# Kernel optimization log

Measured on AMD Instinct MI355X. Metric: run time of the kernel, lower is better.

Reference implementation:

```python
import jax, jax.numpy as jnp
import numpy as np


def setup_inputs() -> dict:
    key = jax.random.key(0)
    k1, k2, k3 = jax.random.split(key, 3)
    B, T, D, K = 8, 1024, 384, 4
    z = jax.random.normal(k1, (B, T, D), dtype=jnp.float32)
    gt_dT = jax.random.normal(k2, (B, T, T, K), dtype=jnp.float32)
    sigma = jax.random.uniform(k3, (K,), dtype=jnp.float32, minval=0.25, maxval=1.0)
    return {"z": z, "gt_dT": gt_dT, "sigma": sigma}


def reference(z, gt_dT, sigma):
    # Pairwise squared distances via ||a-b||^2 = ||a||^2 + ||b||^2 - 2 a.b
    # (same math as the naive [B,T,T,D] expansion, without materializing it).
    sq = jnp.sum(z * z, axis=-1)                      # [B, T]
    gram = jnp.einsum("btd,bsd->bts", z, z)           # [B, T, T]
    dist2 = sq[:, :, None] + sq[:, None, :] - 2.0 * gram
    # Gaussian kernel weight from ground-truth patch-transform deltas.
    kernel = jnp.sum(gt_dT * gt_dT / (2.0 * sigma * sigma), axis=-1)  # [B, T, T]
    w = jnp.exp(-kernel)
    loss = jnp.mean(w * dist2)
    return loss
```

## Files before the change

### kernel.cpp

```cpp
#include <hip/hip_runtime.h>
#include <hip/hip_bf16.h>


typedef float  f32x4   __attribute__((ext_vector_type(4)));
typedef short  bf16x8  __attribute__((ext_vector_type(8)));
typedef unsigned short ushort4_t __attribute__((ext_vector_type(4)));

#define T_DIM 1024
#define D_DIM 384
#define BK    192
#define LDK   200

__device__ __forceinline__ unsigned short f32_bf16(float f) {
    unsigned int u = __float_as_uint(f);
    u += 0x7FFFu + ((u >> 16) & 1u);
    return (unsigned short)(u >> 16);
}

__global__ void prep_sq(const float* __restrict__ z, float* __restrict__ sq) {
    int row  = blockIdx.x;
    int lane = threadIdx.x;
    const float* zr = z + (size_t)row * D_DIM;
    float s = 0.f;
#pragma unroll
    for (int q = 0; q < 6; ++q) {
        float x = zr[lane + 64 * q];
        s += x * x;
    }
#pragma unroll
    for (int off = 32; off; off >>= 1) s += __shfl_down(s, off);
    if (lane == 0) sq[row] = s;
}

__launch_bounds__(256, 2)
__global__ void tile_loss(const float* __restrict__ z,
                          const float* __restrict__ gt,
                          const float* __restrict__ sigma,
                          const float* __restrict__ sq,
                          float* __restrict__ partials) {
    __shared__ unsigned short Alds[64 * LDK];
    __shared__ unsigned short Blds[64 * LDK];
    __shared__ float sqA[64], sqB[64], red[4];

    const int bid = blockIdx.x;
    const int b   = bid >> 8;
    const int r8  = bid & 255;
    const int t0  = (r8 >> 4) * 64;
    const int s0  = (r8 & 15) * 64;

    const int tid  = threadIdx.x;
    const int lane = tid & 63, wid = tid >> 6;
    const int wr = wid >> 1, wc = wid & 1;
    const int l15 = lane & 15, lq = lane >> 4;

    float4 g[2][2][4];
#pragma unroll
    for (int mt = 0; mt < 2; ++mt)
#pragma unroll
        for (int nt = 0; nt < 2; ++nt)
#pragma unroll
            for (int r = 0; r < 4; ++r) {
                int t = t0 + wr * 32 + mt * 16 + lq * 4 + r;
                int s = s0 + wc * 32 + nt * 16 + l15;
                g[mt][nt][r] = *(const float4*)(gt +
                    ((((size_t)b << 10) + t) * T_DIM + (size_t)s) * 4);
            }

    if (tid < 64)       sqA[tid]      = sq[(b << 10) + t0 + tid];
    else if (tid < 128) sqB[tid - 64] = sq[(b << 10) + s0 + (tid - 64)];

    const float* Asrc = z + (((size_t)b << 10) + t0) * D_DIM;
    const float* Bsrc = z + (((size_t)b << 10) + s0) * D_DIM;

    f32x4 acc[2][2] = {};

    for (int kc = 0; kc < 2; ++kc) {
        const int k0 = kc * BK;
        for (int i = tid; i < 3072; i += 256) {
            int row = i / 48, c4 = (i % 48) * 4;
            float4 av = *(const float4*)&Asrc[row * D_DIM + k0 + c4];
            float4 bv = *(const float4*)&Bsrc[row * D_DIM + k0 + c4];
            ushort4_t ah = { f32_bf16(av.x), f32_bf16(av.y), f32_bf16(av.z), f32_bf16(av.w) };
            ushort4_t bh = { f32_bf16(bv.x), f32_bf16(bv.y), f32_bf16(bv.z), f32_bf16(bv.w) };
            *(ushort4_t*)&Alds[row * LDK + c4] = ah;
            *(ushort4_t*)&Blds[row * LDK + c4] = bh;
        }
        __syncthreads();
#pragma unroll
        for (int k = 0; k < BK; k += 32) {
            bf16x8 a0 = *(const bf16x8*)&Alds[(wr * 32 +      l15) * LDK + k + lq * 8];
            bf16x8 a1 = *(const bf16x8*)&Alds[(wr * 32 + 16 + l15) * LDK + k + lq * 8];
            bf16x8 b0 = *(const bf16x8*)&Blds[(wc * 32 +      l15) * LDK + k + lq * 8];
            bf16x8 b1 = *(const bf16x8*)&Blds[(wc * 32 + 16 + l15) * LDK + k + lq * 8];
            acc[0][0] = __builtin_amdgcn_mfma_f32_16x16x32_bf16(a0, b0, acc[0][0], 0, 0, 0);
            acc[0][1] = __builtin_amdgcn_mfma_f32_16x16x32_bf16(a0, b1, acc[0][1], 0, 0, 0);
            acc[1][0] = __builtin_amdgcn_mfma_f32_16x16x32_bf16(a1, b0, acc[1][0], 0, 0, 0);
            acc[1][1] = __builtin_amdgcn_mfma_f32_16x16x32_bf16(a1, b1, acc[1][1], 0, 0, 0);
        }
        __syncthreads();
    }

    const float i0 = 0.5f / (sigma[0] * sigma[0]);
    const float i1 = 0.5f / (sigma[1] * sigma[1]);
    const float i2 = 0.5f / (sigma[2] * sigma[2]);
    const float i3 = 0.5f / (sigma[3] * sigma[3]);

    float psum = 0.f;
#pragma unroll
    for (int mt = 0; mt < 2; ++mt)
#pragma unroll
        for (int nt = 0; nt < 2; ++nt)
#pragma unroll
            for (int r = 0; r < 4; ++r) {
                int tloc = wr * 32 + mt * 16 + lq * 4 + r;
                int sloc = wc * 32 + nt * 16 + l15;
                float gram = acc[mt][nt][r];
                float d2 = sqA[tloc] + sqB[sloc] - 2.0f * gram;
                float4 gv = g[mt][nt][r];
                float kv = gv.x * gv.x * i0 + gv.y * gv.y * i1
                         + gv.z * gv.z * i2 + gv.w * gv.w * i3;
                psum += __expf(-kv) * d2;
            }

#pragma unroll
    for (int off = 32; off; off >>= 1) psum += __shfl_down(psum, off);
    if (lane == 0) red[wid] = psum;
    __syncthreads();
    if (tid == 0) partials[bid] = red[0] + red[1] + red[2] + red[3];
}

__global__ void final_reduce(const float* __restrict__ partials, float* __restrict__ out) {
    __shared__ float red[4];
    int tid = threadIdx.x;
    float s = 0.f;
    for (int i = tid; i < 2048; i += 256) s += partials[i];
#pragma unroll
    for (int off = 32; off; off >>= 1) s += __shfl_down(s, off);
    int lane = tid & 63, wid = tid >> 6;
    if (lane == 0) red[wid] = s;
    __syncthreads();
    if (tid == 0) out[0] = (red[0] + red[1] + red[2] + red[3]) * (1.0f / 8388608.0f);
}

extern "C" void kernel_launch(void* const* d_in, const int* in_sizes, int n_in,
                              void* d_out, int out_size, void* d_ws, size_t ws_size,
                              hipStream_t stream) {
    const float* z     = (const float*)d_in[0];
    const float* gt    = (const float*)d_in[1];
    const float* sigma = (const float*)d_in[2];
    float* out = (float*)d_out;

    float* sq       = (float*)d_ws;
    float* partials = sq + 8192;

    prep_sq<<<8192, 64, 0, stream>>>(z, sq);
    tile_loss<<<2048, 256, 0, stream>>>(z, gt, sigma, sq, partials);
    final_reduce<<<1, 256, 0, stream>>>(partials, out);
}
```

Measured before the change: 66.35 us.

## Keep A fragments in registers and stream four B tiles per block

Each block now covers 64 rows of t against 256 columns of s, processed as four 64-column sub-tiles. The A operand is converted to bf16 once and held in registers across all sub-tiles. B tiles are staged into a full-depth, XOR-swizzled LDS buffer, and the next tile's B data and gt_dT values are prefetched while the current epilogue runs. The grid drops from 2048 to 512 blocks to cut redundant A loads and conversions, at the cost of fewer blocks for latency hiding, more registers per thread, and two extra barriers per sub-tile.

```diff
diff --git a/kernel.cpp b/kernel.cpp
--- a/kernel.cpp
+++ b/kernel.cpp
@@ -8,8 +8,6 @@
 
 #define T_DIM 1024
 #define D_DIM 384
-#define BK    192
-#define LDK   200
 
 __device__ __forceinline__ unsigned short f32_bf16(float f) {
     unsigned int u = __float_as_uint(f);
@@ -38,93 +36,128 @@
                           const float* __restrict__ sigma,
                           const float* __restrict__ sq,
                           float* __restrict__ partials) {
-    __shared__ unsigned short Alds[64 * LDK];
-    __shared__ unsigned short Blds[64 * LDK];
-    __shared__ float sqA[64], sqB[64], red[4];
+    __shared__ unsigned short Blds[64 * D_DIM];
+    __shared__ float sq_s[T_DIM];
+    __shared__ float red[4];
 
-    const int bid = blockIdx.x;
-    const int b   = bid >> 8;
-    const int r8  = bid & 255;
-    const int t0  = (r8 >> 4) * 64;
-    const int s0  = (r8 & 15) * 64;
+    const int bid   = blockIdx.x;
+    const int b     = bid >> 6;
+    const int tt    = (bid >> 2) & 15;
+    const int sgrp  = bid & 3;
+    const int t0    = tt * 64;
+    const int sbase = sgrp * 256;
 
     const int tid  = threadIdx.x;
-    const int lane = tid & 63, wid = tid >> 6;
-    const int wr = wid >> 1, wc = wid & 1;
-    const int l15 = lane & 15, lq = lane >> 4;
+    const int lane = tid & 63, w = tid >> 6;
+    const int l15  = lane & 15, lq = lane >> 4;
 
-    float4 g[2][2][4];
-#pragma unroll
-    for (int mt = 0; mt < 2; ++mt)
-#pragma unroll
-        for (int nt = 0; nt < 2; ++nt)
-#pragma unroll
-            for (int r = 0; r < 4; ++r) {
-                int t = t0 + wr * 32 + mt * 16 + lq * 4 + r;
-                int s = s0 + wc * 32 + nt * 16 + l15;
-                g[mt][nt][r] = *(const float4*)(gt +
-                    ((((size_t)b << 10) + t) * T_DIM + (size_t)s) * 4);
-            }
-
-    if (tid < 64)       sqA[tid]      = sq[(b << 10) + t0 + tid];
-    else if (tid < 128) sqB[tid - 64] = sq[(b << 10) + s0 + (tid - 64)];
-
-    const float* Asrc = z + (((size_t)b << 10) + t0) * D_DIM;
-    const float* Bsrc = z + (((size_t)b << 10) + s0) * D_DIM;
-
-    f32x4 acc[2][2] = {};
-
-    for (int kc = 0; kc < 2; ++kc) {
-        const int k0 = kc * BK;
-        for (int i = tid; i < 3072; i += 256) {
-            int row = i / 48, c4 = (i % 48) * 4;
-            float4 av = *(const float4*)&Asrc[row * D_DIM + k0 + c4];
-            float4 bv = *(const float4*)&Bsrc[row * D_DIM + k0 + c4];
-            ushort4_t ah = { f32_bf16(av.x), f32_bf16(av.y), f32_bf16(av.z), f32_bf16(av.w) };
-            ushort4_t bh = { f32_bf16(bv.x), f32_bf16(bv.y), f32_bf16(bv.z), f32_bf16(bv.w) };
-            *(ushort4_t*)&Alds[row * LDK + c4] = ah;
-            *(ushort4_t*)&Blds[row * LDK + c4] = bh;
-        }
-        __syncthreads();
-#pragma unroll
-        for (int k = 0; k < BK; k += 32) {
-            bf16x8 a0 = *(const bf16x8*)&Alds[(wr * 32 +      l15) * LDK + k + lq * 8];
-            bf16x8 a1 = *(const bf16x8*)&Alds[(wr * 32 + 16 + l15) * LDK + k + lq * 8];
-            bf16x8 b0 = *(const bf16x8*)&Blds[(wc * 32 +      l15) * LDK + k + lq * 8];
-            bf16x8 b1 = *(const bf16x8*)&Blds[(wc * 32 + 16 + l15) * LDK + k + lq * 8];
-            acc[0][0] = __builtin_amdgcn_mfma_f32_16x16x32_bf16(a0, b0, acc[0][0], 0, 0, 0);
-            acc[0][1] = __builtin_amdgcn_mfma_f32_16x16x32_bf16(a0, b1, acc[0][1], 0, 0, 0);
-            acc[1][0] = __builtin_amdgcn_mfma_f32_16x16x32_bf16(a1, b0, acc[1][0], 0, 0, 0);
-            acc[1][1] = __builtin_amdgcn_mfma_f32_16x16x32_bf16(a1, b1, acc[1][1], 0, 0, 0);
-        }
-        __syncthreads();
-    }
+    const float* zb = z + (size_t)b * T_DIM * D_DIM;
+    char* bb = (char*)Blds;
 
     const float i0 = 0.5f / (sigma[0] * sigma[0]);
     const float i1 = 0.5f / (sigma[1] * sigma[1]);
     const float i2 = 0.5f / (sigma[2] * sigma[2]);
     const float i3 = 0.5f / (sigma[3] * sigma[3]);
 
+    *(float4*)&sq_s[tid * 4] = *(const float4*)&sq[b * T_DIM + tid * 4];
+
+    bf16x8 af[12];
+    {
+        const float* Ar = zb + (size_t)(t0 + w * 16 + l15) * D_DIM + lq * 8;
+#pragma unroll
+        for (int kk = 0; kk < 12; ++kk) {
+            float4 lo = *(const float4*)(Ar + kk * 32);
+            float4 hi = *(const float4*)(Ar + kk * 32 + 4);
+            bf16x8 t;
+            t[0] = (short)f32_bf16(lo.x); t[1] = (short)f32_bf16(lo.y);
+            t[2] = (short)f32_bf16(lo.z); t[3] = (short)f32_bf16(lo.w);
+            t[4] = (short)f32_bf16(hi.x); t[5] = (short)f32_bf16(hi.y);
+            t[6] = (short)f32_bf16(hi.z); t[7] = (short)f32_bf16(hi.w);
+            af[kk] = t;
+        }
+    }
+
+    auto stageB = [&](int s0) {
+#pragma unroll
+        for (int rp = 0; rp < 2; ++rp) {
+            int row = rp * 32 + (tid >> 3);
+            const float* src = zb + (size_t)(s0 + row) * D_DIM + (tid & 7) * 4;
+            int base = row * 768 + (tid & 7) * 8;
+            int sw   = (row & 7) << 4;
+#pragma unroll
+            for (int it = 0; it < 12; ++it) {
+                float4 v = *(const float4*)(src + it * 32);
+                ushort4_t h = { f32_bf16(v.x), f32_bf16(v.y),
+                                f32_bf16(v.z), f32_bf16(v.w) };
+                *(ushort4_t*)(bb + ((base + it * 64) ^ sw)) = h;
+            }
+        }
+    };
+
+    const float* gbase = gt + ((size_t)b << 22);
+    auto loadGT = [&](float4 gg[4][4], int s0) {
+#pragma unroll
+        for (int nt = 0; nt < 4; ++nt)
+#pragma unroll
+            for (int r = 0; r < 4; ++r) {
+                int t = t0 + w * 16 + lq * 4 + r;
+                int s = s0 + nt * 16 + l15;
+                gg[nt][r] = *(const float4*)(gbase + (((size_t)t << 10) + s) * 4);
+            }
+    };
+
+    float4 g[4][4];
+    stageB(sbase);
+    loadGT(g, sbase);
+    __syncthreads();
+
     float psum = 0.f;
 #pragma unroll
-    for (int mt = 0; mt < 2; ++mt)
+    for (int j = 0; j < 4; ++j) {
+        f32x4 acc[4] = {};
 #pragma unroll
-        for (int nt = 0; nt < 2; ++nt)
+        for (int kk = 0; kk < 12; ++kk) {
+#pragma unroll
+            for (int nt = 0; nt < 4; ++nt) {
+                int row = nt * 16 + l15;
+                int off = (row * 768 + kk * 64 + lq * 16) ^ ((row & 7) << 4);
+                bf16x8 bf = *(const bf16x8*)(bb + off);
+                acc[nt] = __builtin_amdgcn_mfma_f32_16x16x32_bf16(af[kk], bf, acc[nt], 0, 0, 0);
+            }
+        }
+        __syncthreads();
+
+        float4 gn[4][4];
+        if (j < 3) {
+            stageB(sbase + (j + 1) * 64);
+            loadGT(gn, sbase + (j + 1) * 64);
+        }
+
+#pragma unroll
+        for (int nt = 0; nt < 4; ++nt)
 #pragma unroll
             for (int r = 0; r < 4; ++r) {
-                int tloc = wr * 32 + mt * 16 + lq * 4 + r;
-                int sloc = wc * 32 + nt * 16 + l15;
-                float gram = acc[mt][nt][r];
-                float d2 = sqA[tloc] + sqB[sloc] - 2.0f * gram;
-                float4 gv = g[mt][nt][r];
+                int tg2 = t0 + w * 16 + lq * 4 + r;
+                int sg2 = sbase + j * 64 + nt * 16 + l15;
+                float d2 = sq_s[tg2] + sq_s[sg2] - 2.0f * acc[nt][r];
+                float4 gv = g[nt][r];
                 float kv = gv.x * gv.x * i0 + gv.y * gv.y * i1
                          + gv.z * gv.z * i2 + gv.w * gv.w * i3;
                 psum += __expf(-kv) * d2;
             }
 
+        if (j < 3) {
+#pragma unroll
+            for (int nt = 0; nt < 4; ++nt)
+#pragma unroll
+                for (int r = 0; r < 4; ++r) g[nt][r] = gn[nt][r];
+            __syncthreads();
+        }
+    }
+
 #pragma unroll
     for (int off = 32; off; off >>= 1) psum += __shfl_down(psum, off);
-    if (lane == 0) red[wid] = psum;
+    if (lane == 0) red[w] = psum;
     __syncthreads();
     if (tid == 0) partials[bid] = red[0] + red[1] + red[2] + red[3];
 }
@@ -132,12 +165,10 @@
 __global__ void final_reduce(const float* __restrict__ partials, float* __restrict__ out) {
     __shared__ float red[4];
     int tid = threadIdx.x;
-    float s = 0.f;
-    for (int i = tid; i < 2048; i += 256) s += partials[i];
+    float s = partials[tid] + partials[tid + 256];
 #pragma unroll
     for (int off = 32; off; off >>= 1) s += __shfl_down(s, off);
-    int lane = tid & 63, wid = tid >> 6;
-    if (lane == 0) red[wid] = s;
+    if ((tid & 63) == 0) red[tid >> 6] = s;
     __syncthreads();
     if (tid == 0) out[0] = (red[0] + red[1] + red[2] + red[3]) * (1.0f / 8388608.0f);
 }
@@ -154,6 +185,6 @@
     float* partials = sq + 8192;
 
     prep_sq<<<8192, 64, 0, stream>>>(z, sq);
-    tile_loss<<<2048, 256, 0, stream>>>(z, gt, sigma, sq, partials);
+    tile_loss<<<512, 256, 0, stream>>>(z, gt, sigma, sq, partials);
     final_reduce<<<1, 256, 0, stream>>>(partials, out);
 }
```

Result: faster. 59.20 us (-10.8%).

## Precompute bf16 z in prep kernel and load MFMA operands directly per wave

Applied to the files above, without the earlier changes.

The prep kernel now also writes a bf16 copy of z, so the tile kernel no longer converts fp32 to bf16 or stages operands through LDS with block-wide barriers. Each wave independently computes a 32x32 tile, reading its MFMA fragments straight from global or L2. gt_dT is loaded with nontemporal loads after the GEMM in an interleaved load and consume schedule, exp is replaced by exp2 with log2e folded into the scales, and partials are reduced per wave. The trade is lost A/B reuse across waves in LDS, more global traffic for z, and an extra write pass for the bf16 copy.

```diff
diff --git a/kernel.cpp b/kernel.cpp
--- a/kernel.cpp
+++ b/kernel.cpp
@@ -4,12 +4,9 @@
 
 typedef float  f32x4   __attribute__((ext_vector_type(4)));
 typedef short  bf16x8  __attribute__((ext_vector_type(8)));
-typedef unsigned short ushort4_t __attribute__((ext_vector_type(4)));
 
 #define T_DIM 1024
 #define D_DIM 384
-#define BK    192
-#define LDK   200
 
 __device__ __forceinline__ unsigned short f32_bf16(float f) {
     unsigned int u = __float_as_uint(f);
@@ -17,15 +14,18 @@
     return (unsigned short)(u >> 16);
 }
 
-__global__ void prep_sq(const float* __restrict__ z, float* __restrict__ sq) {
+__global__ void prep(const float* __restrict__ z, float* __restrict__ sq,
+                     unsigned short* __restrict__ zbf) {
     int row  = blockIdx.x;
     int lane = threadIdx.x;
     const float* zr = z + (size_t)row * D_DIM;
+    unsigned short* zo = zbf + (size_t)row * D_DIM;
     float s = 0.f;
 #pragma unroll
     for (int q = 0; q < 6; ++q) {
         float x = zr[lane + 64 * q];
         s += x * x;
+        zo[lane + 64 * q] = f32_bf16(x);
     }
 #pragma unroll
     for (int off = 32; off; off >>= 1) s += __shfl_down(s, off);
@@ -33,111 +33,92 @@
 }
 
 __launch_bounds__(256, 2)
-__global__ void tile_loss(const float* __restrict__ z,
+__global__ void tile_loss(const unsigned short* __restrict__ zbf,
                           const float* __restrict__ gt,
                           const float* __restrict__ sigma,
                           const float* __restrict__ sq,
                           float* __restrict__ partials) {
-    __shared__ unsigned short Alds[64 * LDK];
-    __shared__ unsigned short Blds[64 * LDK];
-    __shared__ float sqA[64], sqB[64], red[4];
+    const int tid  = threadIdx.x;
+    const int lane = tid & 63;
+    const int wid  = blockIdx.x * 4 + (tid >> 6);
+    const int b    = wid >> 10;
+    const int t0   = ((wid >> 5) & 31) * 32;
+    const int s0   = (wid & 31) * 32;
+    const int l15  = lane & 15, lq = lane >> 4;
 
-    const int bid = blockIdx.x;
-    const int b   = bid >> 8;
-    const int r8  = bid & 255;
-    const int t0  = (r8 >> 4) * 64;
-    const int s0  = (r8 & 15) * 64;
+    const float LOG2E = 1.4426950408889634f;
+    const float i0 = LOG2E * 0.5f / (sigma[0] * sigma[0]);
+    const float i1 = LOG2E * 0.5f / (sigma[1] * sigma[1]);
+    const float i2 = LOG2E * 0.5f / (sigma[2] * sigma[2]);
+    const float i3 = LOG2E * 0.5f / (sigma[3] * sigma[3]);
 
-    const int tid  = threadIdx.x;
-    const int lane = tid & 63, wid = tid >> 6;
-    const int wr = wid >> 1, wc = wid & 1;
-    const int l15 = lane & 15, lq = lane >> 4;
+    const float* sqb = sq + b * T_DIM;
+    float4 sqt0 = *(const float4*)&sqb[t0 + lq * 4];
+    float4 sqt1 = *(const float4*)&sqb[t0 + 16 + lq * 4];
+    float  sqs0 = sqb[s0 + l15];
+    float  sqs1 = sqb[s0 + 16 + l15];
 
-    float4 g[2][2][4];
+    const char* zB = (const char*)(zbf + (size_t)b * T_DIM * D_DIM);
+    f32x4 acc00 = {}, acc01 = {}, acc10 = {}, acc11 = {};
 #pragma unroll
-    for (int mt = 0; mt < 2; ++mt)
-#pragma unroll
-        for (int nt = 0; nt < 2; ++nt)
-#pragma unroll
-            for (int r = 0; r < 4; ++r) {
-                int t = t0 + wr * 32 + mt * 16 + lq * 4 + r;
-                int s = s0 + wc * 32 + nt * 16 + l15;
-                g[mt][nt][r] = *(const float4*)(gt +
-                    ((((size_t)b << 10) + t) * T_DIM + (size_t)s) * 4);
-            }
-
-    if (tid < 64)       sqA[tid]      = sq[(b << 10) + t0 + tid];
-    else if (tid < 128) sqB[tid - 64] = sq[(b << 10) + s0 + (tid - 64)];
-
-    const float* Asrc = z + (((size_t)b << 10) + t0) * D_DIM;
-    const float* Bsrc = z + (((size_t)b << 10) + s0) * D_DIM;
-
-    f32x4 acc[2][2] = {};
-
-    for (int kc = 0; kc < 2; ++kc) {
-        const int k0 = kc * BK;
-        for (int i = tid; i < 3072; i += 256) {
-            int row = i / 48, c4 = (i % 48) * 4;
-            float4 av = *(const float4*)&Asrc[row * D_DIM + k0 + c4];
-            float4 bv = *(const float4*)&Bsrc[row * D_DIM + k0 + c4];
-            ushort4_t ah = { f32_bf16(av.x), f32_bf16(av.y), f32_bf16(av.z), f32_bf16(av.w) };
-            ushort4_t bh = { f32_bf16(bv.x), f32_bf16(bv.y), f32_bf16(bv.z), f32_bf16(bv.w) };
-            *(ushort4_t*)&Alds[row * LDK + c4] = ah;
-            *(ushort4_t*)&Blds[row * LDK + c4] = bh;
-        }
-        __syncthreads();
-#pragma unroll
-        for (int k = 0; k < BK; k += 32) {
-            bf16x8 a0 = *(const bf16x8*)&Alds[(wr * 32 +      l15) * LDK + k + lq * 8];
-            bf16x8 a1 = *(const bf16x8*)&Alds[(wr * 32 + 16 + l15) * LDK + k + lq * 8];
-            bf16x8 b0 = *(const bf16x8*)&Blds[(wc * 32 +      l15) * LDK + k + lq * 8];
-            bf16x8 b1 = *(const bf16x8*)&Blds[(wc * 32 + 16 + l15) * LDK + k + lq * 8];
-            acc[0][0] = __builtin_amdgcn_mfma_f32_16x16x32_bf16(a0, b0, acc[0][0], 0, 0, 0);
-            acc[0][1] = __builtin_amdgcn_mfma_f32_16x16x32_bf16(a0, b1, acc[0][1], 0, 0, 0);
-            acc[1][0] = __builtin_amdgcn_mfma_f32_16x16x32_bf16(a1, b0, acc[1][0], 0, 0, 0);
-            acc[1][1] = __builtin_amdgcn_mfma_f32_16x16x32_bf16(a1, b1, acc[1][1], 0, 0, 0);
-        }
-        __syncthreads();
+    for (int kk = 0; kk < 12; ++kk) {
+        const int co = kk * 64 + lq * 16;
+        bf16x8 a0 = *(const bf16x8*)(zB + (size_t)(t0 + l15)      * 768 + co);
+        bf16x8 a1 = *(const bf16x8*)(zB + (size_t)(t0 + 16 + l15) * 768 + co);
+        bf16x8 b0 = *(const bf16x8*)(zB + (size_t)(s0 + l15)      * 768 + co);
+        bf16x8 b1 = *(const bf16x8*)(zB + (size_t)(s0 + 16 + l15) * 768 + co);
+        acc00 = __builtin_amdgcn_mfma_f32_16x16x32_bf16(a0, b0, acc00, 0, 0, 0);
+        acc01 = __builtin_amdgcn_mfma_f32_16x16x32_bf16(a0, b1, acc01, 0, 0, 0);
+        acc10 = __builtin_amdgcn_mfma_f32_16x16x32_bf16(a1, b0, acc10, 0, 0, 0);
+        acc11 = __builtin_amdgcn_mfma_f32_16x16x32_bf16(a1, b1, acc11, 0, 0, 0);
     }
 
-    const float i0 = 0.5f / (sigma[0] * sigma[0]);
-    const float i1 = 0.5f / (sigma[1] * sigma[1]);
-    const float i2 = 0.5f / (sigma[2] * sigma[2]);
-    const float i3 = 0.5f / (sigma[3] * sigma[3]);
+    const float* gbase = gt + ((size_t)b << 22);
+
+#define LOADC(Q, mt, nt)                                                        \
+    _Pragma("unroll")                                                           \
+    for (int r = 0; r < 4; ++r)                                                 \
+        Q[r] = __builtin_nontemporal_load((const f32x4*)(gbase +                \
+            (((size_t)(t0 + (mt) * 16 + lq * 4 + r) << 10) + (s0 + (nt) * 16 + l15)) * 4));
+
+#define CONSC(Q, ACC, SQT, SQS)                                                 \
+    _Pragma("unroll")                                                           \
+    for (int r = 0; r < 4; ++r) {                                               \
+        float d2_ = SQT[r] + SQS - 2.0f * ACC[r];                               \
+        f32x4 g_ = Q[r];                                                        \
+        float kv_ = g_.x * g_.x * i0 + g_.y * g_.y * i1                         \
+                  + g_.z * g_.z * i2 + g_.w * g_.w * i3;                        \
+        psum += exp2f(-kv_) * d2_;                                              \
+    }
 
     float psum = 0.f;
-#pragma unroll
-    for (int mt = 0; mt < 2; ++mt)
-#pragma unroll
-        for (int nt = 0; nt < 2; ++nt)
-#pragma unroll
-            for (int r = 0; r < 4; ++r) {
-                int tloc = wr * 32 + mt * 16 + lq * 4 + r;
-                int sloc = wc * 32 + nt * 16 + l15;
-                float gram = acc[mt][nt][r];
-                float d2 = sqA[tloc] + sqB[sloc] - 2.0f * gram;
-                float4 gv = g[mt][nt][r];
-                float kv = gv.x * gv.x * i0 + gv.y * gv.y * i1
-                         + gv.z * gv.z * i2 + gv.w * gv.w * i3;
-                psum += __expf(-kv) * d2;
-            }
+    f32x4 q0[4], q1[4];
+    LOADC(q0, 0, 0)
+    LOADC(q1, 0, 1)
+    CONSC(q0, acc00, sqt0, sqs0)
+    LOADC(q0, 1, 0)
+    CONSC(q1, acc01, sqt0, sqs1)
+    LOADC(q1, 1, 1)
+    CONSC(q0, acc10, sqt1, sqs0)
+    CONSC(q1, acc11, sqt1, sqs1)
+
+#undef LOADC
+#undef CONSC
 
 #pragma unroll
     for (int off = 32; off; off >>= 1) psum += __shfl_down(psum, off);
-    if (lane == 0) red[wid] = psum;
-    __syncthreads();
-    if (tid == 0) partials[bid] = red[0] + red[1] + red[2] + red[3];
+    if (lane == 0) partials[wid] = psum;
 }
 
 __global__ void final_reduce(const float* __restrict__ partials, float* __restrict__ out) {
     __shared__ float red[4];
     int tid = threadIdx.x;
     float s = 0.f;
-    for (int i = tid; i < 2048; i += 256) s += partials[i];
+#pragma unroll
+    for (int i = 0; i < 32; ++i) s += partials[tid + (i << 8)];
 #pragma unroll
     for (int off = 32; off; off >>= 1) s += __shfl_down(s, off);
-    int lane = tid & 63, wid = tid >> 6;
-    if (lane == 0) red[wid] = s;
+    if ((tid & 63) == 0) red[tid >> 6] = s;
     __syncthreads();
     if (tid == 0) out[0] = (red[0] + red[1] + red[2] + red[3]) * (1.0f / 8388608.0f);
 }
@@ -150,10 +131,11 @@
     const float* sigma = (const float*)d_in[2];
     float* out = (float*)d_out;
 
-    float* sq       = (float*)d_ws;
-    float* partials = sq + 8192;
+    float* sq            = (float*)d_ws;
+    float* partials      = sq + 8192;
+    unsigned short* zbf  = (unsigned short*)(sq + 16384);
 
-    prep_sq<<<8192, 64, 0, stream>>>(z, sq);
-    tile_loss<<<2048, 256, 0, stream>>>(z, gt, sigma, sq, partials);
+    prep<<<8192, 64, 0, stream>>>(z, sq, zbf);
+    tile_loss<<<2048, 256, 0, stream>>>(zbf, gt, sigma, sq, partials);
     final_reduce<<<1, 256, 0, stream>>>(partials, out);
 }
```

Result: slower. 77.39 us (+16.7%).
